# Optimization experiments

Hardware: AMD Instinct MI355X
Metric: run time of the kernel (lower is better)

The kernel has to match this reference:

```python
import jax, jax.numpy as jnp
import numpy as np

DIM = 1024
INTER = 512
E = 32            # n_routed_experts
TOPK = 4          # n_activated_experts
GROUPS = 8        # n_expert_groups
TOPK_GROUPS = 4
SHARED_INTER = 2 * INTER  # n_shared_experts * moe_inter_dim
ROUTE_SCALE = 1.0
B, S = 8, 4096


def setup_inputs() -> dict:
    key = jax.random.key(0)
    ks = jax.random.split(key, 16)
    def xav(k, shape):
        fan_in, fan_out = shape[-2], shape[-1]
        lim = np.sqrt(6.0 / (fan_in + fan_out))
        return jax.random.uniform(k, shape, jnp.float32, -lim, lim)
    return {
        "x": jax.random.normal(ks[0], (B, S, DIM), jnp.float32),
        "gw": xav(ks[1], (DIM, E)),
        "gb": jnp.zeros((E,), jnp.float32),
        "w1": xav(ks[2], (E, DIM, INTER)),
        "b1": jnp.zeros((E, INTER), jnp.float32),
        "w3": xav(ks[3], (E, DIM, INTER)),
        "b3": jnp.zeros((E, INTER), jnp.float32),
        "w2": xav(ks[4], (E, INTER, DIM)),
        "b2": jnp.zeros((E, DIM), jnp.float32),
        "sw1": xav(ks[5], (DIM, SHARED_INTER)),
        "sb1": jnp.zeros((SHARED_INTER,), jnp.float32),
        "sw3": xav(ks[6], (DIM, SHARED_INTER)),
        "sb3": jnp.zeros((SHARED_INTER,), jnp.float32),
        "sw2": xav(ks[7], (SHARED_INTER, DIM)),
        "sb2": jnp.zeros((DIM,), jnp.float32),
    }


def _gate(xf, gw, gb):
    # scores: softmax over routed experts in fp32 (score_func='softmax')
    T = xf.shape[0]
    scores = jax.nn.softmax((xf @ gw + gb).astype(jnp.float32), axis=-1)  # [T, E]
    original_scores = scores
    # group-masked routing (n_expert_groups > 1)
    scores_g = scores.reshape(T, GROUPS, E // GROUPS)                     # [T, G, E/G]
    group_scores = jnp.sum(jax.lax.top_k(scores_g, 2)[0], axis=-1)        # [T, G]
    gidx = jax.lax.top_k(group_scores, TOPK_GROUPS)[1]                    # [T, topk_groups]
    keep = jnp.zeros((T, GROUPS), bool).at[jnp.arange(T)[:, None], gidx].set(True)
    masked = jnp.where(keep[:, :, None], scores_g, -jnp.inf).reshape(T, E)
    indices = jax.lax.top_k(masked, TOPK)[1]                              # [T, topk]
    weights = jnp.take_along_axis(original_scores, indices, axis=1) * ROUTE_SCALE
    return weights.astype(xf.dtype), indices


def reference(x, gw, gb, w1, b1, w3, b3, w2, b2, sw1, sb1, sw3, sb3, sw2, sb2):
    shape = x.shape
    xf = x.reshape(-1, DIM)                                               # [T, dim]
    T = xf.shape[0]
    weights, indices = _gate(xf, gw, gb)
    # dense combine weights [T, E]: w_e(t) = routing weight if expert e chosen for t else 0
    cw = jnp.zeros((T, E), xf.dtype).at[jnp.arange(T)[:, None], indices].add(weights)
    # scan over experts: y += w_e * SwiGLU_e(x). Zero weight -> zero contribution,
    # identical math to the masked dispatch/scatter-add in the torch code.
    def body(y, p):
        w1e, b1e, w3e, b3e, w2e, b2e, we = p
        h = jax.nn.silu(xf @ w1e + b1e) * (xf @ w3e + b3e)                # [T, inter]
        return y + we[:, None] * (h @ w2e + b2e), None
    y0 = jnp.zeros_like(xf)
    y, _ = jax.lax.scan(body, y0, (w1, b1, w3, b3, w2, b2, cw.T))
    # shared experts MLP (SwiGLU)
    z = (jax.nn.silu(xf @ sw1 + sb1) * (xf @ sw3 + sb3)) @ sw2 + sb2
    return (y + z).reshape(shape)
```

## Files before the change

### kernel.cpp

```cpp
#include <hip/hip_runtime.h>
#include <stdint.h>

#define DIM_    1024
#define INTER_  512

typedef short bf16x4 __attribute__((ext_vector_type(4)));
typedef short bf16x8 __attribute__((ext_vector_type(8)));
typedef float f32x4  __attribute__((ext_vector_type(4)));

__device__ __forceinline__ unsigned short f2bf(float f) {
  union { float f; unsigned u; } v; v.f = f;
  return (unsigned short)((v.u + 0x7FFFu + ((v.u >> 16) & 1u)) >> 16);
}
__device__ __forceinline__ unsigned f2bf2(float a, float b) {
  union { float f; unsigned u; } va, vb; va.f = a; vb.f = b;
  unsigned ra = (va.u + 0x7FFFu + ((va.u >> 16) & 1u)) >> 16;
  unsigned rb = (vb.u + 0x7FFFu + ((vb.u >> 16) & 1u)) >> 16;
  return ra | (rb << 16);
}
__device__ __forceinline__ float bfhi(unsigned u) {
  union { unsigned u; float f; } v; v.u = u & 0xffff0000u; return v.f;
}
__device__ __forceinline__ float bflo(unsigned u) {
  union { unsigned u; float f; } v; v.u = u << 16; return v.f;
}

__device__ __forceinline__ void gl16(const void* g, void* l) {
  __builtin_amdgcn_global_load_lds(
      (const __attribute__((address_space(1))) unsigned int*)g,
      (__attribute__((address_space(3))) unsigned int*)l, 16, 0, 0);
}

#define BARX() do { asm volatile("" ::: "memory"); \
                    __builtin_amdgcn_s_barrier();  \
                    asm volatile("" ::: "memory"); } while (0)

__device__ __forceinline__ void gate_body(
    int bI, const float* __restrict__ x, const float* __restrict__ gw,
    const float* __restrict__ gb, int* __restrict__ idx, float* __restrict__ wts,
    unsigned short* __restrict__ xb) {
  const int wid = threadIdx.x >> 6, lane = threadIdx.x & 63;
  const int t = bI * 4 + wid;
  {
    const float* xrow = x + (size_t)t * DIM_ + lane * 16;
    unsigned short* xbrow = xb + (size_t)t * DIM_ + lane * 16;
    float4 f0 = *(const float4*)(xrow);
    float4 f1 = *(const float4*)(xrow + 4);
    float4 f2v = *(const float4*)(xrow + 8);
    float4 f3v = *(const float4*)(xrow + 12);
    uint4 o0, o1;
    o0.x = f2bf2(f0.x, f0.y);  o0.y = f2bf2(f0.z, f0.w);
    o0.z = f2bf2(f1.x, f1.y);  o0.w = f2bf2(f1.z, f1.w);
    o1.x = f2bf2(f2v.x, f2v.y); o1.y = f2bf2(f2v.z, f2v.w);
    o1.z = f2bf2(f3v.x, f3v.y); o1.w = f2bf2(f3v.z, f3v.w);
    *(uint4*)(xbrow) = o0;
    *(uint4*)(xbrow + 8) = o1;
  }
  const int e = lane & 31, half = lane >> 5;
  const float* xr  = x  + (size_t)t * DIM_ + half * 512;
  const float* gwp = gw + (size_t)half * 512 * 32 + e;
  double a0 = 0, a1 = 0, a2 = 0, a3 = 0;
  for (int k = 0; k < 512; k += 4) {
    float4 xv = *(const float4*)(xr + k);
    a0 += (double)xv.x * (double)gwp[(k + 0) * 32];
    a1 += (double)xv.y * (double)gwp[(k + 1) * 32];
    a2 += (double)xv.z * (double)gwp[(k + 2) * 32];
    a3 += (double)xv.w * (double)gwp[(k + 3) * 32];
  }
  double lg = (a0 + a1) + (a2 + a3);
  lg += __shfl_xor(lg, 32);
  lg += (double)gb[e];
  double m = lg;
  #pragma unroll
  for (int d = 1; d < 32; d <<= 1) m = fmax(m, __shfl_xor(m, d));
  double ex = exp(lg - m);
  double ssum = ex;
  #pragma unroll
  for (int d = 1; d < 32; d <<= 1) ssum += __shfl_xor(ssum, d);
  double sc = ex / ssum;
  double p  = __shfl_xor(sc, 1);
  double m1 = fmax(sc, p), n1 = fmin(sc, p);
  double m2 = __shfl_xor(m1, 2), n2 = __shfl_xor(n1, 2);
  double gs = (m1 >= m2) ? (m1 + fmax(n1, m2)) : (m2 + fmax(n2, m1));
  const int gg = lane & 7;
  double gv = __shfl(gs, gg * 4);
  unsigned kmask = 0;
  #pragma unroll
  for (int it = 0; it < 4; ++it) {
    double v = gv; int i = gg;
    #pragma unroll
    for (int d = 1; d < 8; d <<= 1) {
      double vo = __shfl_xor(v, d);
      int io = __shfl_xor(i, d);
      if (vo > v || (vo == v && io < i)) { v = vo; i = io; }
    }
    kmask |= 1u << i;
    if (gg == i) gv = -3.0;
  }
  double ev = ((kmask >> (e >> 2)) & 1u) ? sc : -3.0;
  #pragma unroll
  for (int s = 0; s < 4; ++s) {
    double v = ev; int i = e;
    #pragma unroll
    for (int d = 1; d < 32; d <<= 1) {
      double vo = __shfl_xor(v, d);
      int io = __shfl_xor(i, d);
      if (vo > v || (vo == v && io < i)) { v = vo; i = io; }
    }
    if (lane == 0) { idx[t * 4 + s] = i; wts[t * 4 + s] = (float)v; }
    if (e == i) ev = -3.0;
  }
}

__device__ __forceinline__ void repack_body(
    int bI, const float* __restrict__ src, unsigned short* __restrict__ dst,
    int K, int N, int tilesPerMat) {
  const int w = bI * 4 + (threadIdx.x >> 6);
  const int j = threadIdx.x & 63;
  const int e = w / tilesPerMat, rem = w % tilesPerMat;
  const int kSteps = K >> 5;
  const int nt = rem / kSteps, kq = rem % kSteps;
  const float* s = src + (size_t)e * K * N + (size_t)(kq * 32) * N + nt * 64 + j;
  float v[32];
  #pragma unroll
  for (int kk = 0; kk < 32; ++kk) v[kk] = s[(size_t)kk * N];
  char* d = (char*)dst + (size_t)w * 4096 + j * 16;
  #pragma unroll
  for (int q = 0; q < 4; ++q) {
    int o = q * 8;
    uint4 tv;
    tv.x = f2bf2(v[o + 0], v[o + 1]);
    tv.y = f2bf2(v[o + 2], v[o + 3]);
    tv.z = f2bf2(v[o + 4], v[o + 5]);
    tv.w = f2bf2(v[o + 6], v[o + 7]);
    *(uint4*)(d + q * 1024) = tv;
  }
}

__device__ __forceinline__ void repack13_body(
    int bI, const float* __restrict__ src1, const float* __restrict__ src3,
    unsigned short* __restrict__ dst, int K, int N, int jtTiles) {
  const int w = bI * 4 + (threadIdx.x >> 6);
  const int j = threadIdx.x & 63;
  const int kSteps = K >> 5;
  const int tpm = jtTiles * kSteps;
  const int e = w / tpm, rem = w % tpm;
  const int jt = rem / kSteps, kq = rem % kSteps;
  const int jg = jt * 64 + j;
  const int c = ((jg >> 5) << 4) + (jg & 15);
  const float* s = (((jg >> 4) & 1) ? src3 : src1)
                 + (size_t)e * K * N + (size_t)(kq * 32) * N + c;
  float v[32];
  #pragma unroll
  for (int kk = 0; kk < 32; ++kk) v[kk] = s[(size_t)kk * N];
  char* d = (char*)dst + (size_t)w * 4096 + j * 16;
  #pragma unroll
  for (int q = 0; q < 4; ++q) {
    int o = q * 8;
    uint4 tv;
    tv.x = f2bf2(v[o + 0], v[o + 1]);
    tv.y = f2bf2(v[o + 2], v[o + 3]);
    tv.z = f2bf2(v[o + 4], v[o + 5]);
    tv.w = f2bf2(v[o + 6], v[o + 7]);
    *(uint4*)(d + q * 1024) = tv;
  }
}

#define G4_PRE()                                                              \
  const int tid = threadIdx.x, lane = tid & 63, wave = tid >> 6;              \
  const int wm = wave >> 1, wn = wave & 1;                                    \
  const int f = lane & 15, g = lane >> 4;                                     \
  const int rsg = wave * 16 + (lane >> 2);                                    \
  const int qs = (((lane & 3) ^ ((rsg & 3) ^ ((rsg >> 2) & 3))) << 4);        \
  const int wv1k = wave * 1024;                                               \
  const int bso = (wave & 3) * 1024 + lane * 16;                              \
  int aoff[4], boff[4];                                                       \
  _Pragma("unroll")                                                           \
  for (int ii = 0; ii < 4; ++ii) {                                            \
    int u16 = ii * 16 + f;                                                    \
    aoff[ii] = (wm >> 1) * 8192 + (wm & 1) * 4096 + u16 * 64 +                \
               ((g ^ ((u16 & 3) ^ ((u16 >> 2) & 3))) << 4);                   \
    boff[ii] = 16384 + wn * 4096 + g * 1024 + u16 * 16;                       \
  }                                                                           \
  f32x4 acc[4][4];                                                            \
  const f32x4 zz = {0.f, 0.f, 0.f, 0.f};                                      \
  _Pragma("unroll")                                                           \
  for (int mi = 0; mi < 4; ++mi)                                              \
    _Pragma("unroll")                                                         \
    for (int ni = 0; ni < 4; ++ni) acc[mi][ni] = zz;

#define G4_STAGE(td, u_)                                                      \
  gl16(pA0 + (u_) * 64, (td) + wv1k);                                         \
  gl16(pA1 + (u_) * 64, (td) + 8192 + wv1k);                                  \
  gl16(pB + (size_t)(u_) * 4096, (td) + 16384 + wv1k);

#define G4_BODY(NU)                                                           \
  {                                                                           \
    G4_STAGE(lds, 0);                                                         \
    G4_STAGE(lds + 24576, ((NU) > 1 ? 1 : 0));                                \
    asm volatile("s_waitcnt vmcnt(3)" ::: "memory");                          \
    BARX();                                                                   \
  }                                                                           \
  int bc = 0, bt = 49152;                                                     \
  for (int u = 0; u < (NU); ++u) {                                            \
    int u_ = u + 2; if (u_ > (NU) - 1) u_ = (NU) - 1;                         \
    char* td = lds + bt;                                                      \
    G4_STAGE(td, u_);                                                         \
    const char* cb = lds + bc;                                                \
    bf16x8 af[4], bv[4];                                                      \
    _Pragma("unroll")                                                         \
    for (int mi = 0; mi < 4; ++mi) af[mi] = *(const bf16x8*)(cb + aoff[mi]);  \
    _Pragma("unroll")                                                         \
    for (int ni = 0; ni < 4; ++ni) bv[ni] = *(const bf16x8*)(cb + boff[ni]);  \
    __builtin_amdgcn_s_setprio(1);                                            \
    _Pragma("unroll")                                                         \
    for (int ni = 0; ni < 4; ++ni)                                            \
      _Pragma("unroll")                                                       \
      for (int mi = 0; mi < 4; ++mi)                                          \
        acc[mi][ni] = __builtin_amdgcn_mfma_f32_16x16x32_bf16(                \
            af[mi], bv[ni], acc[mi][ni], 0, 0, 0);                            \
    __builtin_amdgcn_s_setprio(0);                                            \
    asm volatile("s_waitcnt vmcnt(3)" ::: "memory");                          \
    BARX();                                                                   \
    bc = (bc == 49152) ? 0 : bc + 24576;                                      \
    bt = (bt == 49152) ? 0 : bt + 24576;                                      \
  }

__device__ __forceinline__ int2 xcd_swz(int id, int nb, int gx) {
  int w = (id & 7) * (nb >> 3) + (id >> 3);
  int2 r; r.x = w % gx; r.y = w / gx; return r;
}

__device__ __forceinline__ void s1_body(int bx, int by,
    const unsigned short* __restrict__ xb, const unsigned short* __restrict__ w13,
    const float* __restrict__ sb1, const float* __restrict__ sb3,
    unsigned short* __restrict__ Hs, char* lds) {
  const int m0 = by * 256;
  G4_PRE();
  const char* pA0 = (const char*)xb + (size_t)(m0 + rsg) * 2048 + qs;
  const char* pA1 = pA0 + (size_t)128 * 2048;
  const char* pB = (const char*)w13 + ((size_t)(bx * 2 + (wave >> 2)) * 32) * 4096 + bso;
  G4_BODY(32);
  const int colb = bx * 64;
  #pragma unroll
  for (int p2 = 0; p2 < 2; ++p2) {
    int c = colb + wn * 32 + p2 * 16 + f;
    float bb1 = sb1[c], bb3 = sb3[c];
    #pragma unroll
    for (int mi = 0; mi < 4; ++mi) {
      int row = m0 + wm * 64 + mi * 16 + g * 4;
      #pragma unroll
      for (int r = 0; r < 4; ++r) {
        float v1 = acc[mi][2 * p2][r] + bb1;
        float v3 = acc[mi][2 * p2 + 1][r] + bb3;
        float h = (v1 / (1.f + __expf(-v1))) * v3;
        Hs[(size_t)(row + r) * 1024 + c] = f2bf(h);
      }
    }
  }
}

__device__ __forceinline__ void s2_body(int bx, int by,
    const unsigned short* __restrict__ Hs, const unsigned short* __restrict__ b2i,
    const float* __restrict__ sb2, float* __restrict__ out, char* lds) {
  const int m0 = by * 256;
  G4_PRE();
  const char* pA0 = (const char*)Hs + (size_t)(m0 + rsg) * 2048 + qs;
  const char* pA1 = pA0 + (size_t)128 * 2048;
  const char* pB = (const char*)b2i + ((size_t)(bx * 2 + (wave >> 2)) * 32) * 4096 + bso;
  G4_BODY(32);
  #pragma unroll
  for (int ni = 0; ni < 4; ++ni) {
    int c = bx * 128 + wn * 64 + ni * 16 + f;
    float bb = sb2[c];
    #pragma unroll
    for (int mi = 0; mi < 4; ++mi) {
      int row = m0 + wm * 64 + mi * 16 + g * 4;
      #pragma unroll
      for (int r = 0; r < 4; ++r)
        out[(size_t)(row + r) * 1024 + c] = acc[mi][ni][r] + bb;
    }
  }
}

__device__ __forceinline__ void g1_body(int bx, int by,
    const unsigned short* __restrict__ xb, const unsigned short* __restrict__ w13,
    const float* __restrict__ b1, const float* __restrict__ b3,
    const int* __restrict__ tok, const int* __restrict__ meta,
    unsigned short* __restrict__ H, char* lds) {
  if (by >= meta[97]) return;
  const int e = meta[128 + by], m0 = meta[1184 + by];
  const int off_e = meta[64 + e], nrem = meta[e] - m0;
  G4_PRE();
  const int ix0 = off_e + m0 + ((rsg < nrem) ? rsg : 0);
  const int ix1 = off_e + m0 + ((rsg + 128 < nrem) ? rsg + 128 : 0);
  const char* pA0 = (const char*)xb + (size_t)tok[ix0] * 2048 + qs;
  const char* pA1 = (const char*)xb + (size_t)tok[ix1] * 2048 + qs;
  const char* pB = (const char*)w13 + ((size_t)(e * 16 + bx * 2 + (wave >> 2)) * 32) * 4096 + bso;
  G4_BODY(32);
  const int colb = bx * 64;
  #pragma unroll
  for (int p2 = 0; p2 < 2; ++p2) {
    int c = colb + wn * 32 + p2 * 16 + f;
    float bb1 = b1[e * 512 + c], bb3 = b3[e * 512 + c];
    #pragma unroll
    for (int mi = 0; mi < 4; ++mi) {
      int row = wm * 64 + mi * 16 + g * 4;
      #pragma unroll
      for (int r = 0; r < 4; ++r) {
        if (row + r < nrem) {
          float v1 = acc[mi][2 * p2][r] + bb1;
          float v3 = acc[mi][2 * p2 + 1][r] + bb3;
          float h = (v1 / (1.f + __expf(-v1))) * v3;
          H[(size_t)(off_e + m0 + row + r) * 512 + c] = f2bf(h);
        }
      }
    }
  }
}

__device__ __forceinline__ void g2_body(int bx, int by,
    const unsigned short* __restrict__ H, const unsigned short* __restrict__ w2i,
    const float* __restrict__ b2, const int* __restrict__ meta,
    unsigned short* __restrict__ Y, int cbase, char* lds) {
  if (by >= meta[97]) return;
  const int e = meta[128 + by], m0 = meta[1184 + by];
  const int off_e = meta[64 + e], nrem = meta[e] - m0;
  G4_PRE();
  const int ix0 = off_e + m0 + ((rsg < nrem) ? rsg : 0);
  const int ix1 = off_e + m0 + ((rsg + 128 < nrem) ? rsg + 128 : 0);
  const char* pA0 = (const char*)H + (size_t)ix0 * 1024 + qs;
  const char* pA1 = (const char*)H + (size_t)ix1 * 1024 + qs;
  const int nt0 = (cbase >> 6) + bx * 2;
  const char* pB = (const char*)w2i + ((size_t)(e * 16 + nt0 + (wave >> 2)) * 16) * 4096 + bso;
  G4_BODY(16);
  #pragma unroll
  for (int ni = 0; ni < 4; ++ni) {
    int ycol = bx * 128 + wn * 64 + ni * 16 + f;
    float bb = b2[e * 1024 + cbase + ycol];
    #pragma unroll
    for (int mi = 0; mi < 4; ++mi) {
      int row = wm * 64 + mi * 16 + g * 4;
      #pragma unroll
      for (int r = 0; r < 4; ++r) {
        if (row + r < nrem)
          Y[(size_t)(off_e + m0 + row + r) * 512 + ycol] = f2bf(acc[mi][ni][r] + bb);
      }
    }
  }
}

__global__ __launch_bounds__(256) void prep_kernel(
    const float* x, const float* gw, const float* gb, int* idx, float* wts,
    unsigned short* xb,
    const float* w1, const float* w3, unsigned short* w13i,
    const float* w2, unsigned short* w2i,
    const float* sw1, const float* sw3, unsigned short* s13i,
    const float* sw2, unsigned short* sw2i) {
  int b = blockIdx.x;
  if (b < 8192) { gate_body(b, x, gw, gb, idx, wts, xb); return; }
  b -= 8192;
  if (b < 4096) { repack13_body(b, w1, w3, w13i, 1024, 512, 16); return; }
  b -= 4096;
  if (b < 2048) { repack_body(b, w2, w2i, 512, 1024, 256); return; }
  b -= 2048;
  if (b < 256) { repack13_body(b, sw1, sw3, s13i, 1024, 1024, 32); return; }
  b -= 256;
  repack_body(b, sw2, sw2i, 1024, 1024, 512);
}

__global__ __launch_bounds__(256) void count_kernel(const int* __restrict__ idx,
                                                    int* __restrict__ meta) {
  __shared__ int h[32];
  int tid = threadIdx.x;
  if (tid < 32) h[tid] = 0;
  __syncthreads();
  atomicAdd(&h[idx[blockIdx.x * 256 + tid]], 1);
  __syncthreads();
  if (tid < 32 && h[tid]) atomicAdd(&meta[tid], h[tid]);
}

__global__ void scan_kernel(int* __restrict__ meta) {
  int lane = threadIdx.x & 63;
  if (lane < 32) {
    int c = meta[lane];
    int pre = c;
    #pragma unroll
    for (int d = 1; d < 32; d <<= 1) { int t = __shfl_up(pre, d); if (lane >= d) pre += t; }
    int excl = pre - c;
    meta[64 + lane] = excl;
    meta[32 + lane] = excl;
    int nt = (c + 255) >> 8;
    int ntp = nt;
    #pragma unroll
    for (int d = 1; d < 32; d <<= 1) { int t = __shfl_up(ntp, d); if (lane >= d) ntp += t; }
    int ntExcl = ntp - nt;
    for (int k = 0; k < nt; ++k) { meta[128 + ntExcl + k] = lane; meta[1184 + ntExcl + k] = k << 8; }
    if (lane == 31) { meta[96] = excl + c; meta[97] = ntExcl + nt; }
  }
}

__global__ __launch_bounds__(256) void scatter_kernel(
    const int* __restrict__ idx, int* __restrict__ meta,
    int* __restrict__ tok, int* __restrict__ inv) {
  int i = blockIdx.x * 256 + threadIdx.x;
  int lane = threadIdx.x & 63;
  int e = idx[i];
  unsigned long long m = ~0ull;
  #pragma unroll
  for (int b = 0; b < 5; ++b) {
    unsigned long long vote = __ballot((e >> b) & 1);
    m &= ((e >> b) & 1) ? vote : ~vote;
  }
  int leader = __ffsll((long long)m) - 1;
  int rank = __popcll(m & ((1ull << lane) - 1));
  int base = 0;
  if (lane == leader) base = atomicAdd(&meta[32 + e], (int)__popcll(m));
  base = __shfl(base, leader);
  int p = base + rank;
  tok[p] = i >> 2;
  inv[i] = p;
}

__global__ __launch_bounds__(512, 4) void s1_kernel(
    const unsigned short* xb, const unsigned short* w13,
    const float* sb1, const float* sb3, unsigned short* Hs) {
  __shared__ char lds[73728];
  int2 s = xcd_swz(blockIdx.x, 2048, 16);
  s1_body(s.x, s.y, xb, w13, sb1, sb3, Hs, lds);
}
__global__ __launch_bounds__(512, 4) void s2_kernel(
    const unsigned short* Hs, const unsigned short* b2i,
    const float* sb2, float* out) {
  __shared__ char lds[73728];
  int2 s = xcd_swz(blockIdx.x, 1024, 8);
  s2_body(s.x, s.y, Hs, b2i, sb2, out, lds);
}
__global__ __launch_bounds__(512, 4) void g1_kernel(
    const unsigned short* xb, const unsigned short* w13,
    const float* b1, const float* b3, const int* tok, const int* meta,
    unsigned short* H) {
  __shared__ char lds[73728];
  int2 s = xcd_swz(blockIdx.x, 4352, 8);
  g1_body(s.x, s.y, xb, w13, b1, b3, tok, meta, H, lds);
}
__global__ __launch_bounds__(512, 4) void g2_kernel(
    const unsigned short* H, const unsigned short* w2i,
    const float* b2, const int* meta, unsigned short* Y, int cbase) {
  __shared__ char lds[73728];
  int2 s = xcd_swz(blockIdx.x, 2176, 4);
  g2_body(s.x, s.y, H, w2i, b2, meta, Y, cbase, lds);
}

__global__ __launch_bounds__(512, 4) void s1g1_kernel(
    const unsigned short* xb, const unsigned short* s13,
    const float* sb1, const float* sb3, unsigned short* Hs,
    const unsigned short* w13, const float* b1, const float* b3,
    const int* tok, const int* meta, unsigned short* H) {
  __shared__ char lds[73728];
  int id = blockIdx.x;
  int type, sub;
  if (id < 6144) {
    if (id % 3 == 0) { type = 0; sub = id / 3; }
    else { type = 1; sub = id - id / 3 - 1; }
  } else { type = 1; sub = 4096 + (id - 6144); }
  if (type == 0) {
    int2 s = xcd_swz(sub, 2048, 16);
    s1_body(s.x, s.y, xb, s13, sb1, sb3, Hs, lds);
  } else {
    int2 s = xcd_swz(sub, 4352, 8);
    g1_body(s.x, s.y, xb, w13, b1, b3, tok, meta, H, lds);
  }
}

__global__ __launch_bounds__(512, 4) void s2g2_kernel(
    const unsigned short* Hs, const unsigned short* sw2i, const float* sb2,
    float* out, const unsigned short* H, const unsigned short* w2i,
    const float* b2, const int* meta, unsigned short* Y) {
  __shared__ char lds[73728];
  int id = blockIdx.x;
  int type, sub;
  if (id < 3072) {
    if (id % 3 == 0) { type = 0; sub = id / 3; }
    else { type = 1; sub = id - id / 3 - 1; }
  } else { type = 1; sub = 2048 + (id - 3072); }
  if (type == 0) {
    int2 s = xcd_swz(sub, 1024, 8);
    s2_body(s.x, s.y, Hs, sw2i, sb2, out, lds);
  } else {
    int2 s = xcd_swz(sub, 2176, 4);
    g2_body(s.x, s.y, H, w2i, b2, meta, Y, 0, lds);
  }
}

__global__ __launch_bounds__(256) void combine_kernel(
    const unsigned short* __restrict__ Y, const int* __restrict__ inv,
    const float* __restrict__ wts, float* __restrict__ out, int cbase) {
  int t = blockIdx.x * 2 + (threadIdx.x >> 7);
  int c = (threadIdx.x & 127) * 4;
  int4 iv = *(const int4*)(inv + t * 4);
  float4 wv = *(const float4*)(wts + t * 4);
  float* op = out + (size_t)t * 1024 + cbase + c;
  float4 o = *(float4*)op;
  uint2 u;
  u = *(const uint2*)(Y + (size_t)iv.x * 512 + c);
  o.x += wv.x * bflo(u.x); o.y += wv.x * bfhi(u.x);
  o.z += wv.x * bflo(u.y); o.w += wv.x * bfhi(u.y);
  u = *(const uint2*)(Y + (size_t)iv.y * 512 + c);
  o.x += wv.y * bflo(u.x); o.y += wv.y * bfhi(u.x);
  o.z += wv.y * bflo(u.y); o.w += wv.y * bfhi(u.y);
  u = *(const uint2*)(Y + (size_t)iv.z * 512 + c);
  o.x += wv.z * bflo(u.x); o.y += wv.z * bfhi(u.x);
  o.z += wv.z * bflo(u.y); o.w += wv.z * bfhi(u.y);
  u = *(const uint2*)(Y + (size_t)iv.w * 512 + c);
  o.x += wv.w * bflo(u.x); o.y += wv.w * bfhi(u.x);
  o.z += wv.w * bflo(u.y); o.w += wv.w * bfhi(u.y);
  *(float4*)op = o;
}

extern "C" void kernel_launch(void* const* d_in, const int* in_sizes, int n_in,
                              void* d_out, int out_size, void* d_ws, size_t ws_size,
                              hipStream_t stream) {
  const float* x   = (const float*)d_in[0];
  const float* gw  = (const float*)d_in[1];
  const float* gb  = (const float*)d_in[2];
  const float* w1  = (const float*)d_in[3];
  const float* b1  = (const float*)d_in[4];
  const float* w3  = (const float*)d_in[5];
  const float* b3  = (const float*)d_in[6];
  const float* w2  = (const float*)d_in[7];
  const float* b2  = (const float*)d_in[8];
  const float* sw1 = (const float*)d_in[9];
  const float* sb1 = (const float*)d_in[10];
  const float* sw3 = (const float*)d_in[11];
  const float* sb3 = (const float*)d_in[12];
  const float* sw2 = (const float*)d_in[13];
  const float* sb2 = (const float*)d_in[14];
  float* out = (float*)d_out;
  char* ws = (char*)d_ws;

  const size_t OFF_XB   = 134217728;
  const size_t OFF_W13I = 201326592;
  const size_t OFF_W2I  = 268435456;
  const size_t OFF_S13I = 301989888;
  const size_t OFF_SW2I = 306184192;
  const size_t OFF_IDX  = 308281344;
  const size_t OFF_WTS  = 308805632;
  const size_t OFF_TOK  = 309329920;
  const size_t OFF_INV  = 309854208;
  const size_t OFF_META = 310378496;
  const size_t OFF_HS   = 310394880;
  const size_t NEED_SMALL = OFF_META + 8960;
  const size_t NEED_BIG   = OFF_HS + 67108864;
  if (ws_size < NEED_SMALL) return;
  const bool big = ws_size >= NEED_BIG;

  unsigned short* H    = (unsigned short*)ws;
  unsigned short* xb   = (unsigned short*)(ws + OFF_XB);
  unsigned short* Yb   = (unsigned short*)(ws + OFF_XB);
  unsigned short* w13i = (unsigned short*)(ws + OFF_W13I);
  unsigned short* w2i  = (unsigned short*)(ws + OFF_W2I);
  unsigned short* s13i = (unsigned short*)(ws + OFF_S13I);
  unsigned short* sw2i = (unsigned short*)(ws + OFF_SW2I);
  int*   idx  = (int*)(ws + OFF_IDX);
  float* wts  = (float*)(ws + OFF_WTS);
  int*   tokl = (int*)(ws + OFF_TOK);
  int*   inv  = (int*)(ws + OFF_INV);
  int*   meta = (int*)(ws + OFF_META);
  unsigned short* HsBig = (unsigned short*)(ws + OFF_HS);

  hipMemsetAsync(meta, 0, 128, stream);
  prep_kernel<<<dim3(14720), dim3(256), 0, stream>>>(
      x, gw, gb, idx, wts, xb, w1, w3, w13i, w2, w2i, sw1, sw3, s13i, sw2, sw2i);
  count_kernel<<<dim3(512), dim3(256), 0, stream>>>(idx, meta);
  scan_kernel<<<dim3(1), dim3(64), 0, stream>>>(meta);
  scatter_kernel<<<dim3(512), dim3(256), 0, stream>>>(idx, meta, tokl, inv);

  if (big) {
    s1g1_kernel<<<dim3(6400), dim3(512), 0, stream>>>(
        xb, s13i, sb1, sb3, HsBig, w13i, b1, b3, tokl, meta, H);
    s2g2_kernel<<<dim3(3200), dim3(512), 0, stream>>>(
        HsBig, sw2i, sb2, out, H, w2i, b2, meta, Yb);
    combine_kernel<<<dim3(16384), dim3(256), 0, stream>>>(Yb, inv, wts, out, 0);
    g2_kernel<<<dim3(2176), dim3(512), 0, stream>>>(H, w2i, b2, meta, Yb, 512);
    combine_kernel<<<dim3(16384), dim3(256), 0, stream>>>(Yb, inv, wts, out, 512);
  } else {
    s1_kernel<<<dim3(2048), dim3(512), 0, stream>>>(xb, s13i, sb1, sb3, H);
    s2_kernel<<<dim3(1024), dim3(512), 0, stream>>>(H, sw2i, sb2, out);
    g1_kernel<<<dim3(4352), dim3(512), 0, stream>>>(xb, w13i, b1, b3, tokl, meta, H);
    g2_kernel<<<dim3(2176), dim3(512), 0, stream>>>(H, w2i, b2, meta, Yb, 0);
    combine_kernel<<<dim3(16384), dim3(256), 0, stream>>>(Yb, inv, wts, out, 0);
    g2_kernel<<<dim3(2176), dim3(512), 0, stream>>>(H, w2i, b2, meta, Yb, 512);
    combine_kernel<<<dim3(16384), dim3(256), 0, stream>>>(Yb, inv, wts, out, 512);
  }
}
```

Baseline: 1.326 ms.

## Split expert down-projection into column quarters and overlap with combine

```diff
diff --git a/kernel.cpp b/kernel.cpp
--- a/kernel.cpp
+++ b/kernel.cpp
@@ -322,7 +322,7 @@
 __device__ __forceinline__ void g2_body(int bx, int by,
     const unsigned short* __restrict__ H, const unsigned short* __restrict__ w2i,
     const float* __restrict__ b2, const int* __restrict__ meta,
-    unsigned short* __restrict__ Y, int cbase, char* lds) {
+    unsigned short* __restrict__ Y, int cbase, int ystr, char* lds) {
   if (by >= meta[97]) return;
   const int e = meta[128 + by], m0 = meta[1184 + by];
   const int off_e = meta[64 + e], nrem = meta[e] - m0;
@@ -344,10 +344,35 @@
       #pragma unroll
       for (int r = 0; r < 4; ++r) {
         if (row + r < nrem)
-          Y[(size_t)(off_e + m0 + row + r) * 512 + ycol] = f2bf(acc[mi][ni][r] + bb);
+          Y[(size_t)(off_e + m0 + row + r) * ystr + ycol] = f2bf(acc[mi][ni][r] + bb);
       }
     }
   }
+}
+
+__device__ __forceinline__ void combineq_body(int sub,
+    const unsigned short* __restrict__ Y, const int* __restrict__ inv,
+    const float* __restrict__ wts, float* __restrict__ out, int cbase) {
+  int t = sub * 8 + (threadIdx.x >> 6);
+  int c = (threadIdx.x & 63) * 4;
+  int4 iv = *(const int4*)(inv + t * 4);
+  float4 wv = *(const float4*)(wts + t * 4);
+  float* op = out + (size_t)t * 1024 + cbase + c;
+  float4 o = *(float4*)op;
+  uint2 u;
+  u = *(const uint2*)(Y + (size_t)iv.x * 256 + c);
+  o.x += wv.x * bflo(u.x); o.y += wv.x * bfhi(u.x);
+  o.z += wv.x * bflo(u.y); o.w += wv.x * bfhi(u.y);
+  u = *(const uint2*)(Y + (size_t)iv.y * 256 + c);
+  o.x += wv.y * bflo(u.x); o.y += wv.y * bfhi(u.x);
+  o.z += wv.y * bflo(u.y); o.w += wv.y * bfhi(u.y);
+  u = *(const uint2*)(Y + (size_t)iv.z * 256 + c);
+  o.x += wv.z * bflo(u.x); o.y += wv.z * bfhi(u.x);
+  o.z += wv.z * bflo(u.y); o.w += wv.z * bfhi(u.y);
+  u = *(const uint2*)(Y + (size_t)iv.w * 256 + c);
+  o.x += wv.w * bflo(u.x); o.y += wv.w * bfhi(u.x);
+  o.z += wv.w * bflo(u.y); o.w += wv.w * bfhi(u.y);
+  *(float4*)op = o;
 }
 
 __global__ __launch_bounds__(256) void prep_kernel(
@@ -449,7 +474,7 @@
     const float* b2, const int* meta, unsigned short* Y, int cbase) {
   __shared__ char lds[73728];
   int2 s = xcd_swz(blockIdx.x, 2176, 4);
-  g2_body(s.x, s.y, H, w2i, b2, meta, Y, cbase, lds);
+  g2_body(s.x, s.y, H, w2i, b2, meta, Y, cbase, 512, lds);
 }
 
 __global__ __launch_bounds__(512, 4) void s1g1_kernel(
@@ -473,24 +498,43 @@
   }
 }
 
-__global__ __launch_bounds__(512, 4) void s2g2_kernel(
+__global__ __launch_bounds__(512, 4) void s2g2a_kernel(
     const unsigned short* Hs, const unsigned short* sw2i, const float* sb2,
     float* out, const unsigned short* H, const unsigned short* w2i,
-    const float* b2, const int* meta, unsigned short* Y) {
+    const float* b2, const int* meta, unsigned short* Yq0) {
   __shared__ char lds[73728];
   int id = blockIdx.x;
   int type, sub;
-  if (id < 3072) {
-    if (id % 3 == 0) { type = 0; sub = id / 3; }
-    else { type = 1; sub = id - id / 3 - 1; }
-  } else { type = 1; sub = 2048 + (id - 3072); }
+  if (id < 2048) { type = id & 1; sub = id >> 1; }
+  else { type = 1; sub = 1024 + (id - 2048); }
   if (type == 0) {
     int2 s = xcd_swz(sub, 1024, 8);
     s2_body(s.x, s.y, Hs, sw2i, sb2, out, lds);
   } else {
-    int2 s = xcd_swz(sub, 2176, 4);
-    g2_body(s.x, s.y, H, w2i, b2, meta, Y, 0, lds);
-  }
+    int2 s = xcd_swz(sub, 1088, 2);
+    g2_body(s.x, s.y, H, w2i, b2, meta, Yq0, 0, 256, lds);
+  }
+}
+
+__global__ __launch_bounds__(512, 4) void cg2_kernel(
+    const unsigned short* H, const unsigned short* w2i, const float* b2,
+    const int* meta, unsigned short* Ynext, int cbNext,
+    const unsigned short* Yprev, const int* inv, const float* wts,
+    float* out, int cbPrev) {
+  __shared__ char lds[73728];
+  int id = blockIdx.x;
+  if (id < 1088) {
+    int2 s = xcd_swz(id, 1088, 2);
+    g2_body(s.x, s.y, H, w2i, b2, meta, Ynext, cbNext, 256, lds);
+  } else {
+    combineq_body(id - 1088, Yprev, inv, wts, out, cbPrev);
+  }
+}
+
+__global__ __launch_bounds__(512) void combineq_kernel(
+    const unsigned short* Y, const int* inv, const float* wts,
+    float* out, int cbase) {
+  combineq_body(blockIdx.x, Y, inv, wts, out, cbase);
 }
 
 __global__ __launch_bounds__(256) void combine_kernel(
@@ -558,6 +602,8 @@
   unsigned short* H    = (unsigned short*)ws;
   unsigned short* xb   = (unsigned short*)(ws + OFF_XB);
   unsigned short* Yb   = (unsigned short*)(ws + OFF_XB);
+  unsigned short* Yq0  = (unsigned short*)(ws + OFF_XB);
+  unsigned short* Yq1  = (unsigned short*)(ws + OFF_XB + 67108864);
   unsigned short* w13i = (unsigned short*)(ws + OFF_W13I);
   unsigned short* w2i  = (unsigned short*)(ws + OFF_W2I);
   unsigned short* s13i = (unsigned short*)(ws + OFF_S13I);
@@ -579,11 +625,15 @@
   if (big) {
     s1g1_kernel<<<dim3(6400), dim3(512), 0, stream>>>(
         xb, s13i, sb1, sb3, HsBig, w13i, b1, b3, tokl, meta, H);
-    s2g2_kernel<<<dim3(3200), dim3(512), 0, stream>>>(
-        HsBig, sw2i, sb2, out, H, w2i, b2, meta, Yb);
-    combine_kernel<<<dim3(16384), dim3(256), 0, stream>>>(Yb, inv, wts, out, 0);
-    g2_kernel<<<dim3(2176), dim3(512), 0, stream>>>(H, w2i, b2, meta, Yb, 512);
-    combine_kernel<<<dim3(16384), dim3(256), 0, stream>>>(Yb, inv, wts, out, 512);
+    s2g2a_kernel<<<dim3(2112), dim3(512), 0, stream>>>(
+        HsBig, sw2i, sb2, out, H, w2i, b2, meta, Yq0);
+    cg2_kernel<<<dim3(5184), dim3(512), 0, stream>>>(
+        H, w2i, b2, meta, Yq1, 256, Yq0, inv, wts, out, 0);
+    cg2_kernel<<<dim3(5184), dim3(512), 0, stream>>>(
+        H, w2i, b2, meta, Yq0, 512, Yq1, inv, wts, out, 256);
+    cg2_kernel<<<dim3(5184), dim3(512), 0, stream>>>(
+        H, w2i, b2, meta, Yq1, 768, Yq0, inv, wts, out, 512);
+    combineq_kernel<<<dim3(4096), dim3(512), 0, stream>>>(Yq1, inv, wts, out, 768);
   } else {
     s1_kernel<<<dim3(2048), dim3(512), 0, stream>>>(xb, s13i, sb1, sb3, H);
     s2_kernel<<<dim3(1024), dim3(512), 0, stream>>>(H, sw2i, sb2, out);
```

Result: slower. 1.373 ms (+3.5%).
